# Kernel optimization log

Measured on AMD Instinct MI355X. Metric: run time of the kernel, lower is better.

The kernel has to match this reference:

```python
import jax, jax.numpy as jnp
import numpy as np


def _gcn_conv(x, edge_index, W, b):
    # PyG GCNConv: add self loops, symmetric normalization D^-1/2 (A+I) D^-1/2, then linear.
    N = x.shape[0]
    src, dst = edge_index[0], edge_index[1]
    deg = jax.ops.segment_sum(jnp.ones(src.shape[0], x.dtype), dst, num_segments=N) + 1.0
    dinv = jax.lax.rsqrt(deg)  # [N]
    xw = x @ W  # [N, H]
    msg = xw[src] * (dinv[src] * dinv[dst])[:, None]  # [E, H] gathered messages
    agg = jax.ops.segment_sum(msg, dst, num_segments=N)
    agg = agg + xw * (dinv * dinv)[:, None]  # self-loop contribution
    return agg + b


def setup_inputs() -> dict:
    key = jax.random.key(0)
    ks = jax.random.split(key, 10)
    N, E, R = 100_000, 1_600_000, 10_000
    Cin, H, Cout = 64, 64, 1
    x = jax.random.normal(ks[0], (N, Cin), jnp.float32)
    edge_index = jax.random.randint(ks[1], (2, E), 0, N, dtype=jnp.int32)
    edge_attr = jax.random.normal(ks[2], (E, 2), jnp.float32)
    # contiguous route ranges covering [0, E)
    cuts = jnp.sort(jax.random.randint(ks[3], (R - 1,), 0, E, dtype=jnp.int32))
    starts = jnp.concatenate([jnp.zeros((1,), cuts.dtype), cuts])
    ends = jnp.concatenate([cuts, jnp.full((1,), E, cuts.dtype)])
    route_indices = jnp.stack([starts, ends], axis=1)  # [R, 2]
    W1 = jax.random.normal(ks[4], (Cin, H), jnp.float32) / np.sqrt(Cin)
    b1 = jnp.zeros((H,), jnp.float32)
    W2 = jax.random.normal(ks[5], (H, H), jnp.float32) / np.sqrt(H)
    b2 = jnp.zeros((H,), jnp.float32)
    Wfc = jax.random.normal(ks[6], (H + 2, Cout), jnp.float32) / np.sqrt(H + 2)
    bfc = jnp.zeros((Cout,), jnp.float32)
    return dict(x=x, edge_attr=edge_attr, W1=W1, b1=b1, W2=W2, b2=b2,
                Wfc=Wfc, bfc=bfc, edge_index=edge_index, route_indices=route_indices)


def reference(x, edge_attr, W1, b1, W2, b2, Wfc, bfc, edge_index, route_indices):
    h = jax.nn.relu(_gcn_conv(x, edge_index, W1, b1))
    h = jax.nn.relu(_gcn_conv(h, edge_index, W2, b2))
    src = edge_index[0]
    H = h.shape[1]
    # fc(concat([h[src], edge_attr])) without materializing the concat
    pred = h[src] @ Wfc[:H] + edge_attr @ Wfc[H:] + bfc  # [E, Cout]
    pred = pred.sum(axis=1)  # route_pred sums over all fc outputs
    E = src.shape[0]
    starts, ends = route_indices[:, 0], route_indices[:, 1]
    eidx = jnp.arange(E)
    # map each edge to its route segment (ranges are sorted & contiguous)
    seg = jnp.clip(jnp.searchsorted(starts, eidx, side='right') - 1, 0, starts.shape[0] - 1)
    valid = (eidx >= starts[seg]) & (eidx < ends[seg])
    return jax.ops.segment_sum(jnp.where(valid, pred, 0.0), seg,
                               num_segments=route_indices.shape[0])
```

## Files before the change

kernel.cpp:

```cpp
#include <hip/hip_runtime.h>
#include <hip/hip_bf16.h>

typedef unsigned int uint32;
typedef unsigned short ushort;
typedef __attribute__((ext_vector_type(8))) short bf16x8;
typedef __attribute__((ext_vector_type(4))) float f32x4;

#define CAP 64
#define BSZ 512
#define REGION 16384

__device__ __forceinline__ ushort f2bf(float f) {
    unsigned int u = __float_as_uint(f);
    unsigned int r = (u + 0x7FFFu + ((u >> 16) & 1u)) >> 16;
    return (ushort)r;
}
__device__ __forceinline__ float bf_lo(uint32 v) {
    return __uint_as_float(v << 16);
}
__device__ __forceinline__ float bf_hi(uint32 v) {
    return __uint_as_float(v & 0xFFFF0000u);
}
__device__ __forceinline__ bf16x8 pack8(float4 p, float4 q) {
    bf16x8 r;
    r[0] = (short)f2bf(p.x); r[1] = (short)f2bf(p.y);
    r[2] = (short)f2bf(p.z); r[3] = (short)f2bf(p.w);
    r[4] = (short)f2bf(q.x); r[5] = (short)f2bf(q.y);
    r[6] = (short)f2bf(q.z); r[7] = (short)f2bf(q.w);
    return r;
}

__global__ __launch_bounds__(256) void init_cur(int* __restrict__ cur, int nbkt) {
    int i = blockIdx.x * 256 + threadIdx.x;
    if (i < nbkt) cur[i] = i * REGION;
}

__global__ __launch_bounds__(256) void scatter_k(const int* __restrict__ src,
                                                 const int* __restrict__ dst,
                                                 int* __restrict__ cur,
                                                 uint32* __restrict__ buf,
                                                 int E, int nbkt) {
    __shared__ int lcnt[256];
    __shared__ int lbase[256];
    int t = threadIdx.x;
    if (t < 256) lcnt[t] = 0;
    __syncthreads();

    int base = (blockIdx.x * 256 + t) * 8;
    int s[8], d[8], r[8];
    if (base + 8 <= E) {
        int4 sv0 = *(const int4*)(&src[base]);
        int4 sv1 = *(const int4*)(&src[base + 4]);
        int4 dv0 = *(const int4*)(&dst[base]);
        int4 dv1 = *(const int4*)(&dst[base + 4]);
        s[0] = sv0.x; s[1] = sv0.y; s[2] = sv0.z; s[3] = sv0.w;
        s[4] = sv1.x; s[5] = sv1.y; s[6] = sv1.z; s[7] = sv1.w;
        d[0] = dv0.x; d[1] = dv0.y; d[2] = dv0.z; d[3] = dv0.w;
        d[4] = dv1.x; d[5] = dv1.y; d[6] = dv1.z; d[7] = dv1.w;
    } else {
#pragma unroll
        for (int j = 0; j < 8; ++j) {
            int e = base + j;
            s[j] = (e < E) ? src[e] : 0;
            d[j] = (e < E) ? dst[e] : -1;
        }
    }
#pragma unroll
    for (int j = 0; j < 8; ++j) {
        if (d[j] >= 0) r[j] = atomicAdd(&lcnt[d[j] >> 9], 1);
    }
    __syncthreads();
    if (t < nbkt && lcnt[t] > 0) lbase[t] = atomicAdd(&cur[t], lcnt[t]);
    __syncthreads();
#pragma unroll
    for (int j = 0; j < 8; ++j) {
        if (d[j] >= 0) {
            int bkt = d[j] >> 9;
            int idx = lbase[bkt] + r[j];
            if (idx < (bkt + 1) * REGION)
                buf[idx] = ((uint32)s[j] << 9) | (uint32)(d[j] & (BSZ - 1));
        }
    }
}

__global__ __launch_bounds__(256) void fill_bucket(const uint32* __restrict__ buf,
                                                   const int* __restrict__ cur,
                                                   int* __restrict__ col,
                                                   int* __restrict__ cnt,
                                                   float* __restrict__ dinv,
                                                   int N) {
    __shared__ int lcnt[BSZ];
    int b = blockIdx.x;
    int t = threadIdx.x;
    for (int i = t; i < BSZ; i += 256) lcnt[i] = 0;
    __syncthreads();

    int base = b * REGION;
    int end = cur[b];
    int cap = base + REGION;
    if (end > cap) end = cap;
    int node0 = b << 9;
    for (int i = base + t; i < end; i += 256) {
        uint32 u = buf[i];
        int d = (int)(u & (BSZ - 1));
        int s = (int)(u >> 9);
        int slot = atomicAdd(&lcnt[d], 1);
        if (slot < CAP) col[(size_t)(node0 + d) * CAP + slot] = s;
    }
    __syncthreads();
    for (int d = t; d < BSZ; d += 256) {
        int gd = node0 + d;
        if (gd < N) {
            int c = lcnt[d];
            cnt[gd] = c;
            dinv[gd] = rsqrtf((float)c + 1.0f);
        }
    }
}

__global__ __launch_bounds__(256) void prep_w(const float* __restrict__ W1,
                                              const float* __restrict__ W2,
                                              ushort* __restrict__ wb1,
                                              ushort* __restrict__ wb2) {
    int idx = blockIdx.x * 256 + threadIdx.x;
    int e = idx & 7;
    int lane = (idx >> 3) & 63;
    int kk = (idx >> 9) & 1;
    int colT = (idx >> 10) & 3;
    int k = kk * 32 + (lane >> 4) * 8 + e;
    int cc = colT * 16 + (lane & 15);
    wb1[idx] = f2bf(W1[k * 64 + cc]);
    wb2[idx] = f2bf(W2[k * 64 + cc]);
}

__global__ __launch_bounds__(256) void gemm_mfma_x(const float* __restrict__ x,
                                                   const ushort* __restrict__ wb,
                                                   const float* __restrict__ dinv,
                                                   ushort* __restrict__ out, int N) {
    int t = threadIdx.x;
    int w = t >> 6, l = t & 63;
    int row0 = blockIdx.x * 64 + w * 16;
    int lr = l & 15, tq = l >> 4;
    int ar = row0 + lr;
    int arc = ar < N ? ar : N - 1;

    const float* xr = x + (size_t)arc * 64 + tq * 8;
    float4 p0 = *(const float4*)(xr);
    float4 p1 = *(const float4*)(xr + 4);
    float4 q0 = *(const float4*)(xr + 32);
    float4 q1 = *(const float4*)(xr + 36);
    bf16x8 a0 = pack8(p0, p1);
    bf16x8 a1 = pack8(q0, q1);

    const uint4* wb4 = (const uint4*)wb;
    f32x4 acc[4];
#pragma unroll
    for (int c = 0; c < 4; ++c) {
        f32x4 z = {0.f, 0.f, 0.f, 0.f};
        bf16x8 b0 = __builtin_bit_cast(bf16x8, wb4[(c * 2 + 0) * 64 + l]);
        bf16x8 b1 = __builtin_bit_cast(bf16x8, wb4[(c * 2 + 1) * 64 + l]);
        z = __builtin_amdgcn_mfma_f32_16x16x32_bf16(a0, b0, z, 0, 0, 0);
        z = __builtin_amdgcn_mfma_f32_16x16x32_bf16(a1, b1, z, 0, 0, 0);
        acc[c] = z;
    }
#pragma unroll
    for (int r = 0; r < 4; ++r) {
        int g = row0 + tq * 4 + r;
        if (g < N) {
            float dv = dinv[g];
#pragma unroll
            for (int c = 0; c < 4; ++c)
                out[(size_t)g * 64 + c * 16 + lr] = f2bf(acc[c][r] * dv);
        }
    }
}

__global__ __launch_bounds__(256) void gemm_mfma_z(const ushort* __restrict__ zin,
                                                   const ushort* __restrict__ wb,
                                                   ushort* __restrict__ out, int N) {
    int t = threadIdx.x;
    int w = t >> 6, l = t & 63;
    int row0 = blockIdx.x * 64 + w * 16;
    int lr = l & 15, tq = l >> 4;
    int ar = row0 + lr;
    int arc = ar < N ? ar : N - 1;

    const ushort* zr = zin + (size_t)arc * 64 + tq * 8;
    bf16x8 a0 = __builtin_bit_cast(bf16x8, *(const uint4*)(zr));
    bf16x8 a1 = __builtin_bit_cast(bf16x8, *(const uint4*)(zr + 32));

    const uint4* wb4 = (const uint4*)wb;
    f32x4 acc[4];
#pragma unroll
    for (int c = 0; c < 4; ++c) {
        f32x4 z = {0.f, 0.f, 0.f, 0.f};
        bf16x8 b0 = __builtin_bit_cast(bf16x8, wb4[(c * 2 + 0) * 64 + l]);
        bf16x8 b1 = __builtin_bit_cast(bf16x8, wb4[(c * 2 + 1) * 64 + l]);
        z = __builtin_amdgcn_mfma_f32_16x16x32_bf16(a0, b0, z, 0, 0, 0);
        z = __builtin_amdgcn_mfma_f32_16x16x32_bf16(a1, b1, z, 0, 0, 0);
        acc[c] = z;
    }
#pragma unroll
    for (int r = 0; r < 4; ++r) {
        int g = row0 + tq * 4 + r;
        if (g < N) {
#pragma unroll
            for (int c = 0; c < 4; ++c)
                out[(size_t)g * 64 + c * 16 + lr] = f2bf(acc[c][r]);
        }
    }
}

__device__ __forceinline__ void agg_gather8(const uint32* __restrict__ yt,
                                            const int* __restrict__ colrow,
                                            int wid, int nb,
                                            int lane, float acc[8]) {
    int s = lane >> 3;
    int c = lane & 7;
    int cvl = (lane < nb) ? colrow[lane] : -1;
#pragma unroll
    for (int j = 0; j < 8; ++j) acc[j] = 0.f;
    int m = nb + 1;
    int nbat = (m + 7) >> 3;

    auto one = [&](int b) {
        int j = 8 * b + s;
        int sl = j - 1;
        int rr = __shfl(cvl, sl < 0 ? 0 : sl);
        int r = (j == 0) ? wid : ((j >= m) ? -1 : rr);
        if (r >= 0) {
            uint4 v = *(const uint4*)(yt + (size_t)r * 32 + 4 * c);
            acc[0] += bf_lo(v.x); acc[1] += bf_hi(v.x);
            acc[2] += bf_lo(v.y); acc[3] += bf_hi(v.y);
            acc[4] += bf_lo(v.z); acc[5] += bf_hi(v.z);
            acc[6] += bf_lo(v.w); acc[7] += bf_hi(v.w);
        }
    };
    int b = 0;
    for (; b + 3 <= nbat; b += 3) { one(b); one(b + 1); one(b + 2); }
    for (; b < nbat; ++b) one(b);

#pragma unroll
    for (int j = 0; j < 8; ++j) {
        acc[j] += __shfl_xor(acc[j], 8);
        acc[j] += __shfl_xor(acc[j], 16);
        acc[j] += __shfl_xor(acc[j], 32);
    }
}

__global__ __launch_bounds__(256) void agg_z_kernel(const uint32* __restrict__ y1,
                                                    const int* __restrict__ cnt,
                                                    const int* __restrict__ col,
                                                    const float* __restrict__ dinv,
                                                    const float* __restrict__ bias,
                                                    ushort* __restrict__ z,
                                                    int N) {
    int t = threadIdx.x;
    int wid = blockIdx.x * 4 + (t >> 6);
    int lane = t & 63;
    if (wid >= N) return;
    int nb = cnt[wid];
    nb = nb > CAP ? CAP : nb;
    float acc[8];
    agg_gather8(y1, col + (size_t)wid * CAP, wid, nb, lane, acc);

    float di = dinv[wid];
    if (lane < 8) {
        int c = lane;
        float4 bv0 = *(const float4*)(&bias[8 * c]);
        float4 bv1 = *(const float4*)(&bias[8 * c + 4]);
        float h[8];
        h[0] = acc[0] * di + bv0.x; h[1] = acc[1] * di + bv0.y;
        h[2] = acc[2] * di + bv0.z; h[3] = acc[3] * di + bv0.w;
        h[4] = acc[4] * di + bv1.x; h[5] = acc[5] * di + bv1.y;
        h[6] = acc[6] * di + bv1.z; h[7] = acc[7] * di + bv1.w;
        uint32 pk[4];
#pragma unroll
        for (int j = 0; j < 4; ++j) {
            float a = h[2 * j] > 0.f ? h[2 * j] : 0.f;
            float bb = h[2 * j + 1] > 0.f ? h[2 * j + 1] : 0.f;
            pk[j] = (uint32)f2bf(a * di) | ((uint32)f2bf(bb * di) << 16);
        }
        *(uint4*)(&z[(size_t)wid * 64 + 8 * c]) = make_uint4(pk[0], pk[1], pk[2], pk[3]);
    }
}

__global__ __launch_bounds__(256) void agg_nv_kernel(const uint32* __restrict__ y2,
                                                     const int* __restrict__ cnt,
                                                     const int* __restrict__ col,
                                                     const float* __restrict__ dinv,
                                                     const float* __restrict__ bias,
                                                     const float* __restrict__ wfc,
                                                     float* __restrict__ nv, int N) {
    int t = threadIdx.x;
    int wid = blockIdx.x * 4 + (t >> 6);
    int lane = t & 63;
    if (wid >= N) return;
    int c = lane & 7;
    int nb = cnt[wid];
    nb = nb > CAP ? CAP : nb;
    float acc[8];
    agg_gather8(y2, col + (size_t)wid * CAP, wid, nb, lane, acc);

    float di = dinv[wid];
    float4 bv0 = *(const float4*)(&bias[8 * c]);
    float4 bv1 = *(const float4*)(&bias[8 * c + 4]);
    float4 wv0 = *(const float4*)(&wfc[8 * c]);
    float4 wv1 = *(const float4*)(&wfc[8 * c + 4]);
    float p = 0.f, h;
    h = acc[0] * di + bv0.x; p += (h > 0.f ? h : 0.f) * wv0.x;
    h = acc[1] * di + bv0.y; p += (h > 0.f ? h : 0.f) * wv0.y;
    h = acc[2] * di + bv0.z; p += (h > 0.f ? h : 0.f) * wv0.z;
    h = acc[3] * di + bv0.w; p += (h > 0.f ? h : 0.f) * wv0.w;
    h = acc[4] * di + bv1.x; p += (h > 0.f ? h : 0.f) * wv1.x;
    h = acc[5] * di + bv1.y; p += (h > 0.f ? h : 0.f) * wv1.y;
    h = acc[6] * di + bv1.z; p += (h > 0.f ? h : 0.f) * wv1.z;
    h = acc[7] * di + bv1.w; p += (h > 0.f ? h : 0.f) * wv1.w;
    p += __shfl_xor(p, 1);
    p += __shfl_xor(p, 2);
    p += __shfl_xor(p, 4);
    if (lane == 0) nv[wid] = p;
}

__global__ __launch_bounds__(256) void route_kernel(const float* __restrict__ nv,
                                                    const int* __restrict__ src,
                                                    const float* __restrict__ ea,
                                                    const float* __restrict__ wfc,
                                                    const float* __restrict__ bfc,
                                                    const int* __restrict__ routes,
                                                    float* __restrict__ out, int R) {
    int r = blockIdx.x * 4 + (threadIdx.x >> 6);
    int lane = threadIdx.x & 63;
    if (r >= R) return;
    int s0 = routes[2 * r], s1 = routes[2 * r + 1];
    float w0 = wfc[64], w1 = wfc[65], b = bfc[0];
    float acc = 0.f;
    for (int e = s0 + lane; e < s1; e += 64) {
        float2 a = *(const float2*)(&ea[2 * (size_t)e]);
        acc += nv[src[e]] + a.x * w0 + a.y * w1 + b;
    }
#pragma unroll
    for (int off = 32; off; off >>= 1) acc += __shfl_down(acc, off);
    if (lane == 0) out[r] = acc;
}

extern "C" void kernel_launch(void* const* d_in, const int* in_sizes, int n_in,
                              void* d_out, int out_size, void* d_ws, size_t ws_size,
                              hipStream_t stream) {
    const float* x   = (const float*)d_in[0];
    const float* ea  = (const float*)d_in[1];
    const float* W1  = (const float*)d_in[2];
    const float* b1  = (const float*)d_in[3];
    const float* W2  = (const float*)d_in[4];
    const float* b2  = (const float*)d_in[5];
    const float* Wfc = (const float*)d_in[6];
    const float* bfc = (const float*)d_in[7];
    const int* eidx  = (const int*)d_in[8];
    const int* routes= (const int*)d_in[9];

    int N = in_sizes[0] / 64;
    int E = in_sizes[8] / 2;
    int R = in_sizes[9] / 2;
    const int* src = eidx;
    const int* dst = eidx + E;
    int nbkt = (N + BSZ - 1) / BSZ;

    char* ws = (char*)d_ws;
    size_t off = 0;
    auto alloc = [&](size_t bytes) -> void* {
        off = (off + 255) & ~(size_t)255;
        void* p = ws + off;
        off += bytes;
        return p;
    };

    float*  dinv = (float*)alloc((size_t)N * 4);
    int*    cnt  = (int*)alloc((size_t)N * 4);
    int*    cur  = (int*)alloc((size_t)nbkt * 4);
    uint32* buf  = (uint32*)alloc((size_t)nbkt * REGION * 4);
    int*    col  = (int*)alloc((size_t)N * CAP * 4);
    ushort* y1   = (ushort*)alloc((size_t)N * 64 * 2);
    ushort* z    = (ushort*)alloc((size_t)N * 64 * 2);
    float*  nv   = (float*)alloc((size_t)N * 4);
    ushort* wb1  = (ushort*)alloc(4096 * 2);
    ushort* wb2  = (ushort*)alloc(4096 * 2);
    ushort* y2 = y1;

    int eb8 = (E + 2047) / 2048;

    prep_w<<<16, 256, 0, stream>>>(W1, W2, wb1, wb2);

    init_cur<<<(nbkt + 255) / 256, 256, 0, stream>>>(cur, nbkt);
    scatter_k<<<eb8, 256, 0, stream>>>(src, dst, cur, buf, E, nbkt);
    fill_bucket<<<nbkt, 256, 0, stream>>>(buf, cur, col, cnt, dinv, N);

    gemm_mfma_x<<<(N + 63) / 64, 256, 0, stream>>>(x, wb1, dinv, y1, N);
    agg_z_kernel<<<(N + 3) / 4, 256, 0, stream>>>((const uint32*)y1, cnt, col, dinv, b1, z, N);
    gemm_mfma_z<<<(N + 63) / 64, 256, 0, stream>>>(z, wb2, y2, N);
    agg_nv_kernel<<<(N + 3) / 4, 256, 0, stream>>>((const uint32*)y2, cnt, col, dinv, b2, Wfc, nv, N);

    route_kernel<<<(R + 3) / 4, 256, 0, stream>>>(nv, src, ea, Wfc, bfc, routes, (float*)d_out, R);
}
```

Baseline: 180.3 us.

## Fuse second-layer GEMM into aggregation kernel and merge init into weight prep

The layer-1 aggregation kernel now multiplies each node's 64-wide row by W2 directly, using an MFMA with only one valid row per 16, and writes y2. This removes the gemm_mfma_z launch and the z intermediate round-trip through memory. The trade-off is that 15/16 of each MFMA's rows are wasted and there is extra shuffle work per wave. Separately, init_cur is folded into prep_w to save a launch; this relies on nbkt fitting in prep_w's 16*256 threads, which holds at N=100k.

```diff
diff --git a/kernel.cpp b/kernel.cpp
--- a/kernel.cpp
+++ b/kernel.cpp
@@ -30,9 +30,21 @@
     return r;
 }
 
-__global__ __launch_bounds__(256) void init_cur(int* __restrict__ cur, int nbkt) {
-    int i = blockIdx.x * 256 + threadIdx.x;
-    if (i < nbkt) cur[i] = i * REGION;
+__global__ __launch_bounds__(256) void prep_w(const float* __restrict__ W1,
+                                              const float* __restrict__ W2,
+                                              ushort* __restrict__ wb1,
+                                              ushort* __restrict__ wb2,
+                                              int* __restrict__ cur, int nbkt) {
+    int idx = blockIdx.x * 256 + threadIdx.x;
+    if (idx < nbkt) cur[idx] = idx * REGION;
+    int e = idx & 7;
+    int lane = (idx >> 3) & 63;
+    int kk = (idx >> 9) & 1;
+    int colT = (idx >> 10) & 3;
+    int k = kk * 32 + (lane >> 4) * 8 + e;
+    int cc = colT * 16 + (lane & 15);
+    wb1[idx] = f2bf(W1[k * 64 + cc]);
+    wb2[idx] = f2bf(W2[k * 64 + cc]);
 }
 
 __global__ __launch_bounds__(256) void scatter_k(const int* __restrict__ src,
@@ -118,21 +130,6 @@
     }
 }
 
-__global__ __launch_bounds__(256) void prep_w(const float* __restrict__ W1,
-                                              const float* __restrict__ W2,
-                                              ushort* __restrict__ wb1,
-                                              ushort* __restrict__ wb2) {
-    int idx = blockIdx.x * 256 + threadIdx.x;
-    int e = idx & 7;
-    int lane = (idx >> 3) & 63;
-    int kk = (idx >> 9) & 1;
-    int colT = (idx >> 10) & 3;
-    int k = kk * 32 + (lane >> 4) * 8 + e;
-    int cc = colT * 16 + (lane & 15);
-    wb1[idx] = f2bf(W1[k * 64 + cc]);
-    wb2[idx] = f2bf(W2[k * 64 + cc]);
-}
-
 __global__ __launch_bounds__(256) void gemm_mfma_x(const float* __restrict__ x,
                                                    const ushort* __restrict__ wb,
                                                    const float* __restrict__ dinv,
@@ -171,42 +168,6 @@
 #pragma unroll
             for (int c = 0; c < 4; ++c)
                 out[(size_t)g * 64 + c * 16 + lr] = f2bf(acc[c][r] * dv);
-        }
-    }
-}
-
-__global__ __launch_bounds__(256) void gemm_mfma_z(const ushort* __restrict__ zin,
-                                                   const ushort* __restrict__ wb,
-                                                   ushort* __restrict__ out, int N) {
-    int t = threadIdx.x;
-    int w = t >> 6, l = t & 63;
-    int row0 = blockIdx.x * 64 + w * 16;
-    int lr = l & 15, tq = l >> 4;
-    int ar = row0 + lr;
-    int arc = ar < N ? ar : N - 1;
-
-    const ushort* zr = zin + (size_t)arc * 64 + tq * 8;
-    bf16x8 a0 = __builtin_bit_cast(bf16x8, *(const uint4*)(zr));
-    bf16x8 a1 = __builtin_bit_cast(bf16x8, *(const uint4*)(zr + 32));
-
-    const uint4* wb4 = (const uint4*)wb;
-    f32x4 acc[4];
-#pragma unroll
-    for (int c = 0; c < 4; ++c) {
-        f32x4 z = {0.f, 0.f, 0.f, 0.f};
-        bf16x8 b0 = __builtin_bit_cast(bf16x8, wb4[(c * 2 + 0) * 64 + l]);
-        bf16x8 b1 = __builtin_bit_cast(bf16x8, wb4[(c * 2 + 1) * 64 + l]);
-        z = __builtin_amdgcn_mfma_f32_16x16x32_bf16(a0, b0, z, 0, 0, 0);
-        z = __builtin_amdgcn_mfma_f32_16x16x32_bf16(a1, b1, z, 0, 0, 0);
-        acc[c] = z;
-    }
-#pragma unroll
-    for (int r = 0; r < 4; ++r) {
-        int g = row0 + tq * 4 + r;
-        if (g < N) {
-#pragma unroll
-            for (int c = 0; c < 4; ++c)
-                out[(size_t)g * 64 + c * 16 + lr] = f2bf(acc[c][r]);
         }
     }
 }
@@ -248,13 +209,13 @@
     }
 }
 
-__global__ __launch_bounds__(256) void agg_z_kernel(const uint32* __restrict__ y1,
-                                                    const int* __restrict__ cnt,
-                                                    const int* __restrict__ col,
-                                                    const float* __restrict__ dinv,
-                                                    const float* __restrict__ bias,
-                                                    ushort* __restrict__ z,
-                                                    int N) {
+__global__ __launch_bounds__(256) void agg_z2_kernel(const uint32* __restrict__ y1,
+                                                     const int* __restrict__ cnt,
+                                                     const int* __restrict__ col,
+                                                     const float* __restrict__ dinv,
+                                                     const float* __restrict__ bias,
+                                                     const ushort* __restrict__ wb,
+                                                     ushort* __restrict__ y2, int N) {
     int t = threadIdx.x;
     int wid = blockIdx.x * 4 + (t >> 6);
     int lane = t & 63;
@@ -265,23 +226,52 @@
     agg_gather8(y1, col + (size_t)wid * CAP, wid, nb, lane, acc);
 
     float di = dinv[wid];
-    if (lane < 8) {
-        int c = lane;
-        float4 bv0 = *(const float4*)(&bias[8 * c]);
-        float4 bv1 = *(const float4*)(&bias[8 * c + 4]);
-        float h[8];
-        h[0] = acc[0] * di + bv0.x; h[1] = acc[1] * di + bv0.y;
-        h[2] = acc[2] * di + bv0.z; h[3] = acc[3] * di + bv0.w;
-        h[4] = acc[4] * di + bv1.x; h[5] = acc[5] * di + bv1.y;
-        h[6] = acc[6] * di + bv1.z; h[7] = acc[7] * di + bv1.w;
-        uint32 pk[4];
-#pragma unroll
-        for (int j = 0; j < 4; ++j) {
-            float a = h[2 * j] > 0.f ? h[2 * j] : 0.f;
-            float bb = h[2 * j + 1] > 0.f ? h[2 * j + 1] : 0.f;
-            pk[j] = (uint32)f2bf(a * di) | ((uint32)f2bf(bb * di) << 16);
-        }
-        *(uint4*)(&z[(size_t)wid * 64 + 8 * c]) = make_uint4(pk[0], pk[1], pk[2], pk[3]);
+    int c = lane & 7;
+    float4 bv0 = *(const float4*)(&bias[8 * c]);
+    float4 bv1 = *(const float4*)(&bias[8 * c + 4]);
+    float h[8];
+    h[0] = acc[0] * di + bv0.x; h[1] = acc[1] * di + bv0.y;
+    h[2] = acc[2] * di + bv0.z; h[3] = acc[3] * di + bv0.w;
+    h[4] = acc[4] * di + bv1.x; h[5] = acc[5] * di + bv1.y;
+    h[6] = acc[6] * di + bv1.z; h[7] = acc[7] * di + bv1.w;
+    uint32 pk[4];
+#pragma unroll
+    for (int j = 0; j < 4; ++j) {
+        float a = h[2 * j] > 0.f ? h[2 * j] : 0.f;
+        float b = h[2 * j + 1] > 0.f ? h[2 * j + 1] : 0.f;
+        pk[j] = (uint32)f2bf(a * di) | ((uint32)f2bf(b * di) << 16);
+    }
+    int tq = lane >> 4;
+    uint32 a0u[4], a1u[4];
+#pragma unroll
+    for (int j = 0; j < 4; ++j) {
+        a0u[j] = __shfl(pk[j], tq);
+        a1u[j] = __shfl(pk[j], 4 + tq);
+    }
+    bool valid = (lane & 15) == 0;
+#pragma unroll
+    for (int j = 0; j < 4; ++j) {
+        a0u[j] = valid ? a0u[j] : 0u;
+        a1u[j] = valid ? a1u[j] : 0u;
+    }
+    bf16x8 a0 = __builtin_bit_cast(bf16x8, make_uint4(a0u[0], a0u[1], a0u[2], a0u[3]));
+    bf16x8 a1 = __builtin_bit_cast(bf16x8, make_uint4(a1u[0], a1u[1], a1u[2], a1u[3]));
+
+    const uint4* wb4 = (const uint4*)wb;
+    float out4[4];
+#pragma unroll
+    for (int c4 = 0; c4 < 4; ++c4) {
+        f32x4 zz = {0.f, 0.f, 0.f, 0.f};
+        bf16x8 b0 = __builtin_bit_cast(bf16x8, wb4[(c4 * 2 + 0) * 64 + lane]);
+        bf16x8 b1 = __builtin_bit_cast(bf16x8, wb4[(c4 * 2 + 1) * 64 + lane]);
+        zz = __builtin_amdgcn_mfma_f32_16x16x32_bf16(a0, b0, zz, 0, 0, 0);
+        zz = __builtin_amdgcn_mfma_f32_16x16x32_bf16(a1, b1, zz, 0, 0, 0);
+        out4[c4] = zz[0];
+    }
+    if (tq == 0) {
+#pragma unroll
+        for (int c4 = 0; c4 < 4; ++c4)
+            y2[(size_t)wid * 64 + c4 * 16 + lane] = f2bf(out4[c4]);
     }
 }
 
@@ -380,23 +370,20 @@
     uint32* buf  = (uint32*)alloc((size_t)nbkt * REGION * 4);
     int*    col  = (int*)alloc((size_t)N * CAP * 4);
     ushort* y1   = (ushort*)alloc((size_t)N * 64 * 2);
-    ushort* z    = (ushort*)alloc((size_t)N * 64 * 2);
+    ushort* y2   = (ushort*)alloc((size_t)N * 64 * 2);
     float*  nv   = (float*)alloc((size_t)N * 4);
     ushort* wb1  = (ushort*)alloc(4096 * 2);
     ushort* wb2  = (ushort*)alloc(4096 * 2);
-    ushort* y2 = y1;
 
     int eb8 = (E + 2047) / 2048;
 
-    prep_w<<<16, 256, 0, stream>>>(W1, W2, wb1, wb2);
-
-    init_cur<<<(nbkt + 255) / 256, 256, 0, stream>>>(cur, nbkt);
+    prep_w<<<16, 256, 0, stream>>>(W1, W2, wb1, wb2, cur, nbkt);
+
     scatter_k<<<eb8, 256, 0, stream>>>(src, dst, cur, buf, E, nbkt);
     fill_bucket<<<nbkt, 256, 0, stream>>>(buf, cur, col, cnt, dinv, N);
 
     gemm_mfma_x<<<(N + 63) / 64, 256, 0, stream>>>(x, wb1, dinv, y1, N);
-    agg_z_kernel<<<(N + 3) / 4, 256, 0, stream>>>((const uint32*)y1, cnt, col, dinv, b1, z, N);
-    gemm_mfma_z<<<(N + 63) / 64, 256, 0, stream>>>(z, wb2, y2, N);
+    agg_z2_kernel<<<(N + 3) / 4, 256, 0, stream>>>((const uint32*)y1, cnt, col, dinv, b1, wb2, y2, N);
     agg_nv_kernel<<<(N + 3) / 4, 256, 0, stream>>>((const uint32*)y2, cnt, col, dinv, b2, Wfc, nv, N);
 
     route_kernel<<<(R + 3) / 4, 256, 0, stream>>>(nv, src, ea, Wfc, bfc, routes, (float*)d_out, R);
```

Result: no change. 178.2 us (-1.2%).

## Process four nodes per wavefront in aggregation and merge init kernels

Applied to the files above, without the earlier changes.

Aggregation kernels now assign four destination nodes to each wavefront, interleaving their neighbor gathers to raise memory-level parallelism and reduce per-wave overhead. The scatter kernel processes 16 edges per thread instead of 8, and the bucket cursor init is folded into the weight prep kernel to drop one launch. More registers per thread and divergent loop trip counts across the four nodes may lower occupancy or waste lanes.

```diff
diff --git a/kernel.cpp b/kernel.cpp
--- a/kernel.cpp
+++ b/kernel.cpp
@@ -30,9 +30,21 @@
     return r;
 }
 
-__global__ __launch_bounds__(256) void init_cur(int* __restrict__ cur, int nbkt) {
-    int i = blockIdx.x * 256 + threadIdx.x;
-    if (i < nbkt) cur[i] = i * REGION;
+__global__ __launch_bounds__(256) void prep_w(const float* __restrict__ W1,
+                                              const float* __restrict__ W2,
+                                              ushort* __restrict__ wb1,
+                                              ushort* __restrict__ wb2,
+                                              int* __restrict__ cur, int nbkt) {
+    int idx = blockIdx.x * 256 + threadIdx.x;
+    if (idx < nbkt) cur[idx] = idx * REGION;
+    int e = idx & 7;
+    int lane = (idx >> 3) & 63;
+    int kk = (idx >> 9) & 1;
+    int colT = (idx >> 10) & 3;
+    int k = kk * 32 + (lane >> 4) * 8 + e;
+    int cc = colT * 16 + (lane & 15);
+    wb1[idx] = f2bf(W1[k * 64 + cc]);
+    wb2[idx] = f2bf(W2[k * 64 + cc]);
 }
 
 __global__ __launch_bounds__(256) void scatter_k(const int* __restrict__ src,
@@ -46,34 +58,33 @@
     if (t < 256) lcnt[t] = 0;
     __syncthreads();
 
-    int base = (blockIdx.x * 256 + t) * 8;
-    int s[8], d[8], r[8];
-    if (base + 8 <= E) {
-        int4 sv0 = *(const int4*)(&src[base]);
-        int4 sv1 = *(const int4*)(&src[base + 4]);
-        int4 dv0 = *(const int4*)(&dst[base]);
-        int4 dv1 = *(const int4*)(&dst[base + 4]);
-        s[0] = sv0.x; s[1] = sv0.y; s[2] = sv0.z; s[3] = sv0.w;
-        s[4] = sv1.x; s[5] = sv1.y; s[6] = sv1.z; s[7] = sv1.w;
-        d[0] = dv0.x; d[1] = dv0.y; d[2] = dv0.z; d[3] = dv0.w;
-        d[4] = dv1.x; d[5] = dv1.y; d[6] = dv1.z; d[7] = dv1.w;
+    int base = (blockIdx.x * 256 + t) * 16;
+    int s[16], d[16], r[16];
+    if (base + 16 <= E) {
+#pragma unroll
+        for (int q = 0; q < 4; ++q) {
+            int4 sv = *(const int4*)(&src[base + 4 * q]);
+            int4 dv = *(const int4*)(&dst[base + 4 * q]);
+            s[4 * q] = sv.x; s[4 * q + 1] = sv.y; s[4 * q + 2] = sv.z; s[4 * q + 3] = sv.w;
+            d[4 * q] = dv.x; d[4 * q + 1] = dv.y; d[4 * q + 2] = dv.z; d[4 * q + 3] = dv.w;
+        }
     } else {
 #pragma unroll
-        for (int j = 0; j < 8; ++j) {
+        for (int j = 0; j < 16; ++j) {
             int e = base + j;
             s[j] = (e < E) ? src[e] : 0;
             d[j] = (e < E) ? dst[e] : -1;
         }
     }
 #pragma unroll
-    for (int j = 0; j < 8; ++j) {
+    for (int j = 0; j < 16; ++j) {
         if (d[j] >= 0) r[j] = atomicAdd(&lcnt[d[j] >> 9], 1);
     }
     __syncthreads();
     if (t < nbkt && lcnt[t] > 0) lbase[t] = atomicAdd(&cur[t], lcnt[t]);
     __syncthreads();
 #pragma unroll
-    for (int j = 0; j < 8; ++j) {
+    for (int j = 0; j < 16; ++j) {
         if (d[j] >= 0) {
             int bkt = d[j] >> 9;
             int idx = lbase[bkt] + r[j];
@@ -118,21 +129,6 @@
     }
 }
 
-__global__ __launch_bounds__(256) void prep_w(const float* __restrict__ W1,
-                                              const float* __restrict__ W2,
-                                              ushort* __restrict__ wb1,
-                                              ushort* __restrict__ wb2) {
-    int idx = blockIdx.x * 256 + threadIdx.x;
-    int e = idx & 7;
-    int lane = (idx >> 3) & 63;
-    int kk = (idx >> 9) & 1;
-    int colT = (idx >> 10) & 3;
-    int k = kk * 32 + (lane >> 4) * 8 + e;
-    int cc = colT * 16 + (lane & 15);
-    wb1[idx] = f2bf(W1[k * 64 + cc]);
-    wb2[idx] = f2bf(W2[k * 64 + cc]);
-}
-
 __global__ __launch_bounds__(256) void gemm_mfma_x(const float* __restrict__ x,
                                                    const ushort* __restrict__ wb,
                                                    const float* __restrict__ dinv,
@@ -211,40 +207,68 @@
     }
 }
 
-__device__ __forceinline__ void agg_gather8(const uint32* __restrict__ yt,
-                                            const int* __restrict__ colrow,
-                                            int wid, int nb,
-                                            int lane, float acc[8]) {
+__device__ __forceinline__ void agg_gather8_quad(const uint32* __restrict__ yt,
+                                                 const int* __restrict__ col,
+                                                 int wid0, int nbA, int nbB,
+                                                 int nbC, int nbD,
+                                                 int lane,
+                                                 float accA[8], float accB[8],
+                                                 float accC[8], float accD[8]) {
     int s = lane >> 3;
     int c = lane & 7;
-    int cvl = (lane < nb) ? colrow[lane] : -1;
-#pragma unroll
-    for (int j = 0; j < 8; ++j) acc[j] = 0.f;
-    int m = nb + 1;
-    int nbat = (m + 7) >> 3;
-
-    auto one = [&](int b) {
-        int j = 8 * b + s;
-        int sl = j - 1;
-        int rr = __shfl(cvl, sl < 0 ? 0 : sl);
-        int r = (j == 0) ? wid : ((j >= m) ? -1 : rr);
-        if (r >= 0) {
-            uint4 v = *(const uint4*)(yt + (size_t)r * 32 + 4 * c);
-            acc[0] += bf_lo(v.x); acc[1] += bf_hi(v.x);
-            acc[2] += bf_lo(v.y); acc[3] += bf_hi(v.y);
-            acc[4] += bf_lo(v.z); acc[5] += bf_hi(v.z);
-            acc[6] += bf_lo(v.w); acc[7] += bf_hi(v.w);
-        }
-    };
-    int b = 0;
-    for (; b + 3 <= nbat; b += 3) { one(b); one(b + 1); one(b + 2); }
-    for (; b < nbat; ++b) one(b);
+    const int* rA = col + (size_t)(wid0 + 0) * CAP;
+    const int* rB = col + (size_t)(wid0 + 1) * CAP;
+    const int* rC = col + (size_t)(wid0 + 2) * CAP;
+    const int* rD = col + (size_t)(wid0 + 3) * CAP;
+    int cvlA = (lane < nbA) ? rA[lane] : -1;
+    int cvlB = (nbB > 0 && lane < nbB) ? rB[lane] : -1;
+    int cvlC = (nbC > 0 && lane < nbC) ? rC[lane] : -1;
+    int cvlD = (nbD > 0 && lane < nbD) ? rD[lane] : -1;
+#pragma unroll
+    for (int j = 0; j < 8; ++j) { accA[j] = 0.f; accB[j] = 0.f; accC[j] = 0.f; accD[j] = 0.f; }
+    int mA = nbA + 1;
+    int mB = (nbB >= 0) ? nbB + 1 : 0;
+    int mC = (nbC >= 0) ? nbC + 1 : 0;
+    int mD = (nbD >= 0) ? nbD + 1 : 0;
+    int nA = (mA + 7) >> 3, nB = (mB + 7) >> 3, nC = (mC + 7) >> 3, nD = (mD + 7) >> 3;
+    int nbat = nA; if (nB > nbat) nbat = nB; if (nC > nbat) nbat = nC; if (nD > nbat) nbat = nD;
+
+#define ONE(cvl, wid, m, acc)                                            \
+    {                                                                    \
+        int j = 8 * b + s;                                               \
+        int sl = j - 1;                                                  \
+        int rr = __shfl(cvl, sl < 0 ? 0 : sl);                           \
+        int r = (j == 0) ? (wid) : ((j >= (m)) ? -1 : rr);               \
+        if (r >= 0) {                                                    \
+            uint4 v = *(const uint4*)(yt + (size_t)r * 32 + 4 * c);      \
+            acc[0] += bf_lo(v.x); acc[1] += bf_hi(v.x);                  \
+            acc[2] += bf_lo(v.y); acc[3] += bf_hi(v.y);                  \
+            acc[4] += bf_lo(v.z); acc[5] += bf_hi(v.z);                  \
+            acc[6] += bf_lo(v.w); acc[7] += bf_hi(v.w);                  \
+        }                                                                \
+    }
+    for (int b = 0; b < nbat; ++b) {
+        if (b < nA) ONE(cvlA, wid0 + 0, mA, accA);
+        if (b < nB) ONE(cvlB, wid0 + 1, mB, accB);
+        if (b < nC) ONE(cvlC, wid0 + 2, mC, accC);
+        if (b < nD) ONE(cvlD, wid0 + 3, mD, accD);
+    }
+#undef ONE
 
 #pragma unroll
     for (int j = 0; j < 8; ++j) {
-        acc[j] += __shfl_xor(acc[j], 8);
-        acc[j] += __shfl_xor(acc[j], 16);
-        acc[j] += __shfl_xor(acc[j], 32);
+        accA[j] += __shfl_xor(accA[j], 8);
+        accB[j] += __shfl_xor(accB[j], 8);
+        accC[j] += __shfl_xor(accC[j], 8);
+        accD[j] += __shfl_xor(accD[j], 8);
+        accA[j] += __shfl_xor(accA[j], 16);
+        accB[j] += __shfl_xor(accB[j], 16);
+        accC[j] += __shfl_xor(accC[j], 16);
+        accD[j] += __shfl_xor(accD[j], 16);
+        accA[j] += __shfl_xor(accA[j], 32);
+        accB[j] += __shfl_xor(accB[j], 32);
+        accC[j] += __shfl_xor(accC[j], 32);
+        accD[j] += __shfl_xor(accD[j], 32);
     }
 }
 
@@ -253,35 +277,37 @@
                                                     const int* __restrict__ col,
                                                     const float* __restrict__ dinv,
                                                     const float* __restrict__ bias,
-                                                    ushort* __restrict__ z,
-                                                    int N) {
-    int t = threadIdx.x;
-    int wid = blockIdx.x * 4 + (t >> 6);
+                                                    ushort* __restrict__ z, int N) {
+    int t = threadIdx.x;
+    int wid0 = (blockIdx.x * 4 + (t >> 6)) * 4;
     int lane = t & 63;
-    if (wid >= N) return;
-    int nb = cnt[wid];
-    nb = nb > CAP ? CAP : nb;
-    float acc[8];
-    agg_gather8(y1, col + (size_t)wid * CAP, wid, nb, lane, acc);
-
-    float di = dinv[wid];
-    if (lane < 8) {
-        int c = lane;
+    if (wid0 >= N) return;
+    int nbA = cnt[wid0];
+    int nbB = (wid0 + 1 < N) ? cnt[wid0 + 1] : -1;
+    int nbC = (wid0 + 2 < N) ? cnt[wid0 + 2] : -1;
+    int nbD = (wid0 + 3 < N) ? cnt[wid0 + 3] : -1;
+    nbA = nbA > CAP ? CAP : nbA; nbB = nbB > CAP ? CAP : nbB;
+    nbC = nbC > CAP ? CAP : nbC; nbD = nbD > CAP ? CAP : nbD;
+    float accA[8], accB[8], accC[8], accD[8];
+    agg_gather8_quad(y1, col, wid0, nbA, nbB, nbC, nbD, lane, accA, accB, accC, accD);
+
+    int s = lane >> 3, c = lane & 7;
+    int gw = wid0 + s;
+    if (s < 4 && gw < N) {
+        float di = dinv[gw];
         float4 bv0 = *(const float4*)(&bias[8 * c]);
         float4 bv1 = *(const float4*)(&bias[8 * c + 4]);
-        float h[8];
-        h[0] = acc[0] * di + bv0.x; h[1] = acc[1] * di + bv0.y;
-        h[2] = acc[2] * di + bv0.z; h[3] = acc[3] * di + bv0.w;
-        h[4] = acc[4] * di + bv1.x; h[5] = acc[5] * di + bv1.y;
-        h[6] = acc[6] * di + bv1.z; h[7] = acc[7] * di + bv1.w;
+        float bv[8] = {bv0.x, bv0.y, bv0.z, bv0.w, bv1.x, bv1.y, bv1.z, bv1.w};
         uint32 pk[4];
 #pragma unroll
         for (int j = 0; j < 4; ++j) {
-            float a = h[2 * j] > 0.f ? h[2 * j] : 0.f;
-            float bb = h[2 * j + 1] > 0.f ? h[2 * j + 1] : 0.f;
-            pk[j] = (uint32)f2bf(a * di) | ((uint32)f2bf(bb * di) << 16);
-        }
-        *(uint4*)(&z[(size_t)wid * 64 + 8 * c]) = make_uint4(pk[0], pk[1], pk[2], pk[3]);
+            float v0 = (s == 0) ? accA[2 * j] : (s == 1) ? accB[2 * j] : (s == 2) ? accC[2 * j] : accD[2 * j];
+            float v1 = (s == 0) ? accA[2 * j + 1] : (s == 1) ? accB[2 * j + 1] : (s == 2) ? accC[2 * j + 1] : accD[2 * j + 1];
+            float h0 = v0 * di + bv[2 * j];     h0 = h0 > 0.f ? h0 : 0.f;
+            float h1 = v1 * di + bv[2 * j + 1]; h1 = h1 > 0.f ? h1 : 0.f;
+            pk[j] = (uint32)f2bf(h0 * di) | ((uint32)f2bf(h1 * di) << 16);
+        }
+        *(uint4*)(&z[(size_t)gw * 64 + 8 * c]) = make_uint4(pk[0], pk[1], pk[2], pk[3]);
     }
 }
 
@@ -293,33 +319,45 @@
                                                      const float* __restrict__ wfc,
                                                      float* __restrict__ nv, int N) {
     int t = threadIdx.x;
-    int wid = blockIdx.x * 4 + (t >> 6);
+    int wid0 = (blockIdx.x * 4 + (t >> 6)) * 4;
     int lane = t & 63;
-    if (wid >= N) return;
-    int c = lane & 7;
-    int nb = cnt[wid];
-    nb = nb > CAP ? CAP : nb;
-    float acc[8];
-    agg_gather8(y2, col + (size_t)wid * CAP, wid, nb, lane, acc);
-
-    float di = dinv[wid];
+    if (wid0 >= N) return;
+    int nbA = cnt[wid0];
+    int nbB = (wid0 + 1 < N) ? cnt[wid0 + 1] : -1;
+    int nbC = (wid0 + 2 < N) ? cnt[wid0 + 2] : -1;
+    int nbD = (wid0 + 3 < N) ? cnt[wid0 + 3] : -1;
+    nbA = nbA > CAP ? CAP : nbA; nbB = nbB > CAP ? CAP : nbB;
+    nbC = nbC > CAP ? CAP : nbC; nbD = nbD > CAP ? CAP : nbD;
+    float accA[8], accB[8], accC[8], accD[8];
+    agg_gather8_quad(y2, col, wid0, nbA, nbB, nbC, nbD, lane, accA, accB, accC, accD);
+
+    int s = lane >> 3, c = lane & 7;
+    float diA = dinv[wid0];
+    float diB = (nbB >= 0) ? dinv[wid0 + 1] : 0.f;
+    float diC = (nbC >= 0) ? dinv[wid0 + 2] : 0.f;
+    float diD = (nbD >= 0) ? dinv[wid0 + 3] : 0.f;
     float4 bv0 = *(const float4*)(&bias[8 * c]);
     float4 bv1 = *(const float4*)(&bias[8 * c + 4]);
     float4 wv0 = *(const float4*)(&wfc[8 * c]);
     float4 wv1 = *(const float4*)(&wfc[8 * c + 4]);
-    float p = 0.f, h;
-    h = acc[0] * di + bv0.x; p += (h > 0.f ? h : 0.f) * wv0.x;
-    h = acc[1] * di + bv0.y; p += (h > 0.f ? h : 0.f) * wv0.y;
-    h = acc[2] * di + bv0.z; p += (h > 0.f ? h : 0.f) * wv0.z;
-    h = acc[3] * di + bv0.w; p += (h > 0.f ? h : 0.f) * wv0.w;
-    h = acc[4] * di + bv1.x; p += (h > 0.f ? h : 0.f) * wv1.x;
-    h = acc[5] * di + bv1.y; p += (h > 0.f ? h : 0.f) * wv1.y;
-    h = acc[6] * di + bv1.z; p += (h > 0.f ? h : 0.f) * wv1.z;
-    h = acc[7] * di + bv1.w; p += (h > 0.f ? h : 0.f) * wv1.w;
-    p += __shfl_xor(p, 1);
-    p += __shfl_xor(p, 2);
-    p += __shfl_xor(p, 4);
-    if (lane == 0) nv[wid] = p;
+    float bv[8] = {bv0.x, bv0.y, bv0.z, bv0.w, bv1.x, bv1.y, bv1.z, bv1.w};
+    float wv[8] = {wv0.x, wv0.y, wv0.z, wv0.w, wv1.x, wv1.y, wv1.z, wv1.w};
+    float pA = 0.f, pB = 0.f, pC = 0.f, pD = 0.f, h;
+#pragma unroll
+    for (int j = 0; j < 8; ++j) {
+        h = accA[j] * diA + bv[j]; pA += (h > 0.f ? h : 0.f) * wv[j];
+        h = accB[j] * diB + bv[j]; pB += (h > 0.f ? h : 0.f) * wv[j];
+        h = accC[j] * diC + bv[j]; pC += (h > 0.f ? h : 0.f) * wv[j];
+        h = accD[j] * diD + bv[j]; pD += (h > 0.f ? h : 0.f) * wv[j];
+    }
+    pA += __shfl_xor(pA, 1); pB += __shfl_xor(pB, 1); pC += __shfl_xor(pC, 1); pD += __shfl_xor(pD, 1);
+    pA += __shfl_xor(pA, 2); pB += __shfl_xor(pB, 2); pC += __shfl_xor(pC, 2); pD += __shfl_xor(pD, 2);
+    pA += __shfl_xor(pA, 4); pB += __shfl_xor(pB, 4); pC += __shfl_xor(pC, 4); pD += __shfl_xor(pD, 4);
+    int gw = wid0 + s;
+    if (c == 0 && s < 4 && gw < N) {
+        float p = (s == 0) ? pA : (s == 1) ? pB : (s == 2) ? pC : pD;
+        nv[gw] = p;
+    }
 }
 
 __global__ __launch_bounds__(256) void route_kernel(const float* __restrict__ nv,
@@ -386,18 +424,17 @@
     ushort* wb2  = (ushort*)alloc(4096 * 2);
     ushort* y2 = y1;
 
-    int eb8 = (E + 2047) / 2048;
-
-    prep_w<<<16, 256, 0, stream>>>(W1, W2, wb1, wb2);
-
-    init_cur<<<(nbkt + 255) / 256, 256, 0, stream>>>(cur, nbkt);
-    scatter_k<<<eb8, 256, 0, stream>>>(src, dst, cur, buf, E, nbkt);
+    int eb16 = (E + 4095) / 4096;
+
+    prep_w<<<16, 256, 0, stream>>>(W1, W2, wb1, wb2, cur, nbkt);
+
+    scatter_k<<<eb16, 256, 0, stream>>>(src, dst, cur, buf, E, nbkt);
     fill_bucket<<<nbkt, 256, 0, stream>>>(buf, cur, col, cnt, dinv, N);
 
     gemm_mfma_x<<<(N + 63) / 64, 256, 0, stream>>>(x, wb1, dinv, y1, N);
-    agg_z_kernel<<<(N + 3) / 4, 256, 0, stream>>>((const uint32*)y1, cnt, col, dinv, b1, z, N);
+    agg_z_kernel<<<(N + 15) / 16, 256, 0, stream>>>((const uint32*)y1, cnt, col, dinv, b1, z, N);
     gemm_mfma_z<<<(N + 63) / 64, 256, 0, stream>>>(z, wb2, y2, N);
-    agg_nv_kernel<<<(N + 3) / 4, 256, 0, stream>>>((const uint32*)y2, cnt, col, dinv, b2, Wfc, nv, N);
+    agg_nv_kernel<<<(N + 15) / 16, 256, 0, stream>>>((const uint32*)y2, cnt, col, dinv, b2, Wfc, nv, N);
 
     route_kernel<<<(R + 3) / 4, 256, 0, stream>>>(nv, src, ea, Wfc, bfc, routes, (float*)d_out, R);
 }
```

Measured after the change: 182.8 us. Within noise of the previous version (+1.3%).
